# Kernel tuning notes

Hardware: AMD Instinct MI355X
Metric: run time of the kernel (lower is better)

The kernel has to match this reference:

```python
import jax, jax.numpy as jnp
import numpy as np
import math

B, L, H, E = 16, 1024, 8, 64   # L = nsensor = N (forced by einsum 'bhls,bhlg')
WIN = 1024                      # win_size, last dim of x
G = 64                          # n_group
D_SEL = 1                       # d_sel default


def setup_inputs() -> dict:
    key = jax.random.key(0)
    ks = jax.random.split(key, 7)
    return {
        "queries": jax.random.normal(ks[0], (B, L, H, E), dtype=jnp.float32),
        "keys": jax.random.normal(ks[1], (B, L, H, E), dtype=jnp.float32),
        "values": jax.random.normal(ks[2], (B, L, H, E), dtype=jnp.float32),
        "x": jax.random.normal(ks[3], (B, L, WIN), dtype=jnp.float32),
        "mlp_w": jax.random.normal(ks[4], (H * D_SEL, WIN), dtype=jnp.float32) * 0.02,
        "mlp_b": jax.random.normal(ks[5], (H * D_SEL,), dtype=jnp.float32) * 0.02,
        "sel_W": jax.random.normal(ks[6], (H, G, D_SEL), dtype=jnp.float32),
        "attn_mask": 0,
    }


def _select_attention(x, mlp_w, mlp_b, sel_W, n_heads, d_sel):
    b, n, lwin = x.shape
    xf = x.reshape(b * n, lwin)
    newx = jnp.tanh(xf @ mlp_w.T + mlp_b)                 # [(B*N), H*d_sel]
    # Faithful raw reshape (torch.reshape, no permute): mixes n and h axes.
    newx = newx.reshape(b, n_heads, n, d_sel)             # [B, H, N, d_sel]
    sel = jnp.einsum('bhnd,hgd->bhng', newx, sel_W)       # [B, H, N, G]
    return jax.nn.relu(sel)


def reference(queries, keys, values, x, mlp_w, mlp_b, sel_W, attn_mask):
    b, l, h, e = queries.shape
    scale = 1.0 / math.sqrt(e)
    scores = jnp.einsum('blhe,bshe->bhls', queries, keys)      # [B, H, L, S]
    sel = _select_attention(x, mlp_w, mlp_b, sel_W, h, D_SEL)  # [B, H, L, G]
    scores = jnp.einsum('bhls,bhlg->bhsg', scores, sel)        # [B, H, S, G]
    series = jax.nn.softmax(scale * scores, axis=-1)           # softmax over groups
    # values labeled 'blhs': l=S (value len), s=D (feature). Output V: [B, D, H, G]
    V = jnp.einsum('blhs,bhlg->bshg', values, series)
    return V
```

## Files before the change

kernel.cpp:

```cpp
#include <hip/hip_runtime.h>
#include <math.h>

#define NB 16
#define NL 1024
#define NH 8
#define NE 64
#define NWIN 1024
#define NG 64

#define SCH 128
#define SROW 136

typedef __attribute__((ext_vector_type(8))) short short8;
typedef __attribute__((ext_vector_type(4))) float floatx4;

__device__ __forceinline__ short f2bf(float x) {
    unsigned u = __float_as_uint(x);
    u += 0x7fffu + ((u >> 16) & 1u);
    return (short)(u >> 16);
}
__device__ __forceinline__ float dot4(float4 a, float4 b) {
    return fmaf(a.x, b.x, fmaf(a.y, b.y, fmaf(a.z, b.z, a.w * b.w)));
}

__global__ __launch_bounds__(256) void k_sel_q(
    const float* __restrict__ x, const float* __restrict__ mlp_w,
    const float* __restrict__ mlp_b, const float* __restrict__ q,
    float* __restrict__ qp, float* __restrict__ qn)
{
    __shared__ float4 w_lds[8][NWIN / 4];
    __shared__ float t_lds[256];
    __shared__ float redp[4][64], redn[4][64];

    int tid = threadIdx.x;
    int blk = blockIdx.x;
    int qq = blk & 3, bh = blk >> 2;
    int b = bh >> 3, h = bh & 7;
    int w = tid >> 6, lane = tid & 63;

    const float4* w4 = (const float4*)mlp_w;
    float4* wl = (float4*)w_lds;
    #pragma unroll
    for (int i = 0; i < 8; ++i)
        wl[tid + 256 * i] = w4[tid + 256 * i];
    __syncthreads();

    float4 keep03 = make_float4(0,0,0,0), keep47 = make_float4(0,0,0,0);
    int r0 = b * 1024 + h * 128 + qq * 32 + w * 8;
    for (int j = 0; j < 8; ++j) {
        const float4* xr = (const float4*)(x + (size_t)(r0 + j) * NWIN);
        float4 a03 = make_float4(0,0,0,0), a47 = make_float4(0,0,0,0);
        #pragma unroll
        for (int it = 0; it < 4; ++it) {
            float4 xv = xr[it * 64 + lane];
            a03.x += dot4(xv, w_lds[0][it * 64 + lane]);
            a03.y += dot4(xv, w_lds[1][it * 64 + lane]);
            a03.z += dot4(xv, w_lds[2][it * 64 + lane]);
            a03.w += dot4(xv, w_lds[3][it * 64 + lane]);
            a47.x += dot4(xv, w_lds[4][it * 64 + lane]);
            a47.y += dot4(xv, w_lds[5][it * 64 + lane]);
            a47.z += dot4(xv, w_lds[6][it * 64 + lane]);
            a47.w += dot4(xv, w_lds[7][it * 64 + lane]);
        }
        #pragma unroll
        for (int off = 1; off < 64; off <<= 1) {
            a03.x += __shfl_xor(a03.x, off, 64);
            a03.y += __shfl_xor(a03.y, off, 64);
            a03.z += __shfl_xor(a03.z, off, 64);
            a03.w += __shfl_xor(a03.w, off, 64);
            a47.x += __shfl_xor(a47.x, off, 64);
            a47.y += __shfl_xor(a47.y, off, 64);
            a47.z += __shfl_xor(a47.z, off, 64);
            a47.w += __shfl_xor(a47.w, off, 64);
        }
        if (lane == j) { keep03 = a03; keep47 = a47; }
    }
    if (lane < 8) {
        float4 b03 = *(const float4*)mlp_b;
        float4 b47 = *(const float4*)(mlp_b + 4);
        float4 t03, t47;
        t03.x = tanhf(keep03.x + b03.x); t03.y = tanhf(keep03.y + b03.y);
        t03.z = tanhf(keep03.z + b03.z); t03.w = tanhf(keep03.w + b03.w);
        t47.x = tanhf(keep47.x + b47.x); t47.y = tanhf(keep47.y + b47.y);
        t47.z = tanhf(keep47.z + b47.z); t47.w = tanhf(keep47.w + b47.w);
        *(float4*)&t_lds[w * 64 + lane * 8]     = t03;
        *(float4*)&t_lds[w * 64 + lane * 8 + 4] = t47;
    }
    __syncthreads();

    int lo = lane >> 4, e4 = lane & 15;
    float4 accp = make_float4(0,0,0,0), accn = make_float4(0,0,0,0);
    #pragma unroll 4
    for (int i = 0; i < 16; ++i) {
        int l_loc = w * 64 + i * 4 + lo;
        float tv = t_lds[l_loc];
        int l = qq * 256 + l_loc;
        float4 qv = *(const float4*)(q + (((size_t)(b * NL + l)) * NH + h) * NE + e4 * 4);
        float tp = fmaxf(tv, 0.f), tn = fminf(tv, 0.f);
        accp.x = fmaf(tp, qv.x, accp.x); accp.y = fmaf(tp, qv.y, accp.y);
        accp.z = fmaf(tp, qv.z, accp.z); accp.w = fmaf(tp, qv.w, accp.w);
        accn.x = fmaf(tn, qv.x, accn.x); accn.y = fmaf(tn, qv.y, accn.y);
        accn.z = fmaf(tn, qv.z, accn.z); accn.w = fmaf(tn, qv.w, accn.w);
    }
    #pragma unroll
    for (int off = 16; off <= 32; off <<= 1) {
        accp.x += __shfl_xor(accp.x, off, 64); accp.y += __shfl_xor(accp.y, off, 64);
        accp.z += __shfl_xor(accp.z, off, 64); accp.w += __shfl_xor(accp.w, off, 64);
        accn.x += __shfl_xor(accn.x, off, 64); accn.y += __shfl_xor(accn.y, off, 64);
        accn.z += __shfl_xor(accn.z, off, 64); accn.w += __shfl_xor(accn.w, off, 64);
    }
    if (lo == 0) {
        *(float4*)&redp[w][e4 * 4] = accp;
        *(float4*)&redn[w][e4 * 4] = accn;
    }
    __syncthreads();
    if (tid < 64) {
        atomicAdd(&qp[bh * NE + tid], redp[0][tid] + redp[1][tid] + redp[2][tid] + redp[3][tid]);
    } else if (tid < 128) {
        int e = tid - 64;
        atomicAdd(&qn[bh * NE + e], redn[0][e] + redn[1][e] + redn[2][e] + redn[3][e]);
    }
}

__global__ __launch_bounds__(256, 4) void k_attn_out(
    const float* __restrict__ keys, const float* __restrict__ values,
    const float* __restrict__ sel_W,
    const float* __restrict__ qp, const float* __restrict__ qn,
    float* __restrict__ out)
{
    __shared__ short sb[NG][SROW];
    __shared__ float ap_l[SCH], an_l[SCH];
    __shared__ float2 wpn[NG];
    __shared__ float mx2[2][SCH], dn2[2][SCH];

    int tid = threadIdx.x, blk = blockIdx.x;
    int chunk = blk & 7, bh = blk >> 3;
    int b = bh >> 3, h = bh & 7;
    int w = tid >> 6, lane = tid & 63;
    int c = lane & 15, sq = lane >> 4;
    const float scale = 0.125f;

    if (tid < NG) {
        float W = sel_W[h * NG + tid];
        wpn[tid] = make_float2(fmaxf(W, 0.f) * scale, fminf(W, 0.f) * scale);
    }

    const float4 qp4 = *(const float4*)(qp + bh * NE + c * 4);
    const float4 qn4 = *(const float4*)(qn + bh * NE + c * 4);
    int s0 = chunk * SCH;

    #pragma unroll
    for (int p = 0; p < 8; ++p) {
        int sl = w * 32 + p * 4 + sq;
        float4 kv = *(const float4*)(keys + (((size_t)(b * NL + s0 + sl)) * NH + h) * NE + c * 4);
        float pp = dot4(kv, qp4);
        float pn = dot4(kv, qn4);
        #pragma unroll
        for (int m_ = 1; m_ <= 8; m_ <<= 1) {
            pp += __shfl_xor(pp, m_, 64);
            pn += __shfl_xor(pn, m_, 64);
        }
        if (c == 0) { ap_l[sl] = pp; an_l[sl] = pn; }
    }
    __syncthreads();

    {
        int s_ = tid & 127, gh = tid >> 7, g0 = gh * 32;
        float ap = ap_l[s_], an = an_l[s_];
        float m = -1e30f;
        #pragma unroll 8
        for (int g = 0; g < 32; ++g) {
            float2 wv = wpn[g0 + g];
            m = fmaxf(m, fmaf(wv.x, ap, wv.y * an));
        }
        mx2[gh][s_] = m;
        __syncthreads();
        m = fmaxf(mx2[0][s_], mx2[1][s_]);
        float d = 0.f;
        #pragma unroll 8
        for (int g = 0; g < 32; ++g) {
            float2 wv = wpn[g0 + g];
            d += __expf(fmaf(wv.x, ap, wv.y * an) - m);
        }
        dn2[gh][s_] = d;
        __syncthreads();
        float inv = 1.0f / (dn2[0][s_] + dn2[1][s_]);
        #pragma unroll 8
        for (int g = 0; g < 32; ++g) {
            float2 wv = wpn[g0 + g];
            sb[g0 + g][s_] = f2bf(__expf(fmaf(wv.x, ap, wv.y * an) - m) * inv);
        }
    }
    __syncthreads();

    floatx4 acc[4] = {{0.f,0.f,0.f,0.f},{0.f,0.f,0.f,0.f},
                      {0.f,0.f,0.f,0.f},{0.f,0.f,0.f,0.f}};
    const float* vbase = values + (((size_t)(b * NL + s0)) * NH + h) * NE + 16 * w + c;
    #pragma unroll
    for (int ks = 0; ks < 4; ++ks) {
        float a[8];
        #pragma unroll
        for (int j = 0; j < 8; ++j)
            a[j] = vbase[(size_t)(ks * 32 + sq * 8 + j) * (NH * NE)];
        short8 av;
        #pragma unroll
        for (int j = 0; j < 8; ++j) av[j] = f2bf(a[j]);
        #pragma unroll
        for (int n = 0; n < 4; ++n) {
            short8 bv = *(const short8*)&sb[16 * n + c][ks * 32 + sq * 8];
            acc[n] = __builtin_amdgcn_mfma_f32_16x16x32_bf16(av, bv, acc[n], 0, 0, 0);
        }
    }

    #pragma unroll
    for (int n = 0; n < 4; ++n) {
        #pragma unroll
        for (int r = 0; r < 4; ++r) {
            int e = 16 * w + sq * 4 + r;
            int g = 16 * n + c;
            atomicAdd(&out[((size_t)(b * NE + e) * NH + h) * NG + g], acc[n][r]);
        }
    }
}

extern "C" void kernel_launch(void* const* d_in, const int* in_sizes, int n_in,
                              void* d_out, int out_size, void* d_ws, size_t ws_size,
                              hipStream_t stream) {
    (void)in_sizes; (void)n_in; (void)ws_size;
    const float* queries = (const float*)d_in[0];
    const float* keys    = (const float*)d_in[1];
    const float* values  = (const float*)d_in[2];
    const float* x       = (const float*)d_in[3];
    const float* mlp_w   = (const float*)d_in[4];
    const float* mlp_b   = (const float*)d_in[5];
    const float* sel_W   = (const float*)d_in[6];
    float* out = (float*)d_out;

    float* qp_ws = (float*)d_ws;
    float* qn_ws = qp_ws + NB * NH * NE;

    hipMemsetAsync(out, 0, (size_t)out_size * sizeof(float), stream);
    hipMemsetAsync(qp_ws, 0, (size_t)2 * NB * NH * NE * sizeof(float), stream);

    k_sel_q<<<dim3(NB * NH * 4), dim3(256), 0, stream>>>(x, mlp_w, mlp_b,
                                                          queries, qp_ws, qn_ws);
    k_attn_out<<<dim3(NB * NH * 8), dim3(256), 0, stream>>>(keys, values, sel_W,
                                                            qp_ws, qn_ws, out);
}
```

Before: 199.2 us.

## Double grid of selection kernel, prefetch values, replace output atomics with partial-sum reduction

The selection/MLP kernel now launches twice as many blocks, each covering half the rows. It double-buffers x row loads and uses a transpose-style butterfly reduction so each lane ends up with one output instead of reducing all eight. The attention kernel issues its value loads at kernel start to overlap them with the softmax work. It writes per-chunk partial outputs instead of atomically adding to the output, and a new reduce kernel sums the eight chunks. This removes the output memset and atomics but adds a workspace round trip, an extra launch and higher register pressure from 32 prefetched floats.

```diff
diff --git a/kernel.cpp b/kernel.cpp
--- a/kernel.cpp
+++ b/kernel.cpp
@@ -29,12 +29,12 @@
     float* __restrict__ qp, float* __restrict__ qn)
 {
     __shared__ float4 w_lds[8][NWIN / 4];
-    __shared__ float t_lds[256];
+    __shared__ float t_lds[128];
     __shared__ float redp[4][64], redn[4][64];
 
     int tid = threadIdx.x;
     int blk = blockIdx.x;
-    int qq = blk & 3, bh = blk >> 2;
+    int qq = blk & 7, bh = blk >> 3;
     int b = bh >> 3, h = bh & 7;
     int w = tid >> 6, lane = tid & 63;
 
@@ -45,56 +45,63 @@
         wl[tid + 256 * i] = w4[tid + 256 * i];
     __syncthreads();
 
-    float4 keep03 = make_float4(0,0,0,0), keep47 = make_float4(0,0,0,0);
-    int r0 = b * 1024 + h * 128 + qq * 32 + w * 8;
-    for (int j = 0; j < 8; ++j) {
-        const float4* xr = (const float4*)(x + (size_t)(r0 + j) * NWIN);
-        float4 a03 = make_float4(0,0,0,0), a47 = make_float4(0,0,0,0);
+    int r0 = b * 1024 + h * 128 + qq * 16 + w * 4;
+    float bc = mlp_b[lane & 7];
+    float4 xa[4], xb[4];
+    {
+        const float4* p0 = (const float4*)(x + (size_t)r0 * NWIN);
+        #pragma unroll
+        for (int it = 0; it < 4; ++it) xa[it] = p0[it * 64 + lane];
+    }
+    #pragma unroll
+    for (int j = 0; j < 4; ++j) {
+        if (j < 3) {
+            const float4* pn = (const float4*)(x + (size_t)(r0 + j + 1) * NWIN);
+            #pragma unroll
+            for (int it = 0; it < 4; ++it) xb[it] = pn[it * 64 + lane];
+        }
+        float o0=0,o1=0,o2=0,o3=0,o4=0,o5=0,o6=0,o7=0;
         #pragma unroll
         for (int it = 0; it < 4; ++it) {
-            float4 xv = xr[it * 64 + lane];
-            a03.x += dot4(xv, w_lds[0][it * 64 + lane]);
-            a03.y += dot4(xv, w_lds[1][it * 64 + lane]);
-            a03.z += dot4(xv, w_lds[2][it * 64 + lane]);
-            a03.w += dot4(xv, w_lds[3][it * 64 + lane]);
-            a47.x += dot4(xv, w_lds[4][it * 64 + lane]);
-            a47.y += dot4(xv, w_lds[5][it * 64 + lane]);
-            a47.z += dot4(xv, w_lds[6][it * 64 + lane]);
-            a47.w += dot4(xv, w_lds[7][it * 64 + lane]);
-        }
-        #pragma unroll
-        for (int off = 1; off < 64; off <<= 1) {
-            a03.x += __shfl_xor(a03.x, off, 64);
-            a03.y += __shfl_xor(a03.y, off, 64);
-            a03.z += __shfl_xor(a03.z, off, 64);
-            a03.w += __shfl_xor(a03.w, off, 64);
-            a47.x += __shfl_xor(a47.x, off, 64);
-            a47.y += __shfl_xor(a47.y, off, 64);
-            a47.z += __shfl_xor(a47.z, off, 64);
-            a47.w += __shfl_xor(a47.w, off, 64);
-        }
-        if (lane == j) { keep03 = a03; keep47 = a47; }
-    }
-    if (lane < 8) {
-        float4 b03 = *(const float4*)mlp_b;
-        float4 b47 = *(const float4*)(mlp_b + 4);
-        float4 t03, t47;
-        t03.x = tanhf(keep03.x + b03.x); t03.y = tanhf(keep03.y + b03.y);
-        t03.z = tanhf(keep03.z + b03.z); t03.w = tanhf(keep03.w + b03.w);
-        t47.x = tanhf(keep47.x + b47.x); t47.y = tanhf(keep47.y + b47.y);
-        t47.z = tanhf(keep47.z + b47.z); t47.w = tanhf(keep47.w + b47.w);
-        *(float4*)&t_lds[w * 64 + lane * 8]     = t03;
-        *(float4*)&t_lds[w * 64 + lane * 8 + 4] = t47;
-    }
-    __syncthreads();
+            float4 xv = xa[it];
+            o0 += dot4(xv, w_lds[0][it * 64 + lane]);
+            o1 += dot4(xv, w_lds[1][it * 64 + lane]);
+            o2 += dot4(xv, w_lds[2][it * 64 + lane]);
+            o3 += dot4(xv, w_lds[3][it * 64 + lane]);
+            o4 += dot4(xv, w_lds[4][it * 64 + lane]);
+            o5 += dot4(xv, w_lds[5][it * 64 + lane]);
+            o6 += dot4(xv, w_lds[6][it * 64 + lane]);
+            o7 += dot4(xv, w_lds[7][it * 64 + lane]);
+        }
+        o0 += __shfl_xor(o0, 1, 64); o1 += __shfl_xor(o1, 1, 64);
+        o2 += __shfl_xor(o2, 1, 64); o3 += __shfl_xor(o3, 1, 64);
+        o4 += __shfl_xor(o4, 1, 64); o5 += __shfl_xor(o5, 1, 64);
+        o6 += __shfl_xor(o6, 1, 64); o7 += __shfl_xor(o7, 1, 64);
+        bool b0 = lane & 1;
+        float m0 = b0 ? o1 : o0, m1 = b0 ? o3 : o2;
+        float m2 = b0 ? o5 : o4, m3 = b0 ? o7 : o6;
+        m0 += __shfl_xor(m0, 2, 64); m1 += __shfl_xor(m1, 2, 64);
+        m2 += __shfl_xor(m2, 2, 64); m3 += __shfl_xor(m3, 2, 64);
+        bool b1 = lane & 2;
+        float n0 = b1 ? m1 : m0, n1 = b1 ? m3 : m2;
+        n0 += __shfl_xor(n0, 4, 64); n1 += __shfl_xor(n1, 4, 64);
+        float q0 = (lane & 4) ? n1 : n0;
+        q0 += __shfl_xor(q0, 8, 64);
+        q0 += __shfl_xor(q0, 16, 64);
+        q0 += __shfl_xor(q0, 32, 64);
+        if (lane < 8)
+            t_lds[w * 32 + j * 8 + lane] = tanhf(q0 + bc);
+        #pragma unroll
+        for (int it = 0; it < 4; ++it) xa[it] = xb[it];
+    }
 
     int lo = lane >> 4, e4 = lane & 15;
     float4 accp = make_float4(0,0,0,0), accn = make_float4(0,0,0,0);
-    #pragma unroll 4
-    for (int i = 0; i < 16; ++i) {
-        int l_loc = w * 64 + i * 4 + lo;
+    #pragma unroll
+    for (int i = 0; i < 8; ++i) {
+        int l_loc = w * 32 + i * 4 + lo;
         float tv = t_lds[l_loc];
-        int l = qq * 256 + l_loc;
+        int l = qq * 128 + l_loc;
         float4 qv = *(const float4*)(q + (((size_t)(b * NL + l)) * NH + h) * NE + e4 * 4);
         float tp = fmaxf(tv, 0.f), tn = fminf(tv, 0.f);
         accp.x = fmaf(tp, qv.x, accp.x); accp.y = fmaf(tp, qv.y, accp.y);
@@ -126,7 +133,7 @@
     const float* __restrict__ keys, const float* __restrict__ values,
     const float* __restrict__ sel_W,
     const float* __restrict__ qp, const float* __restrict__ qn,
-    float* __restrict__ out)
+    float* __restrict__ partial)
 {
     __shared__ short sb[NG][SROW];
     __shared__ float ap_l[SCH], an_l[SCH];
@@ -139,15 +146,22 @@
     int w = tid >> 6, lane = tid & 63;
     int c = lane & 15, sq = lane >> 4;
     const float scale = 0.125f;
+    int s0 = chunk * SCH;
+
+    float vreg[32];
+    const float* vbase = values + (((size_t)(b * NL + s0)) * NH + h) * NE + 16 * w + c;
+    #pragma unroll
+    for (int ks = 0; ks < 4; ++ks)
+        #pragma unroll
+        for (int j = 0; j < 8; ++j)
+            vreg[ks * 8 + j] = vbase[(size_t)(ks * 32 + sq * 8 + j) * (NH * NE)];
 
     if (tid < NG) {
         float W = sel_W[h * NG + tid];
         wpn[tid] = make_float2(fmaxf(W, 0.f) * scale, fminf(W, 0.f) * scale);
     }
-
     const float4 qp4 = *(const float4*)(qp + bh * NE + c * 4);
     const float4 qn4 = *(const float4*)(qn + bh * NE + c * 4);
-    int s0 = chunk * SCH;
 
     #pragma unroll
     for (int p = 0; p < 8; ++p) {
@@ -195,16 +209,11 @@
 
     floatx4 acc[4] = {{0.f,0.f,0.f,0.f},{0.f,0.f,0.f,0.f},
                       {0.f,0.f,0.f,0.f},{0.f,0.f,0.f,0.f}};
-    const float* vbase = values + (((size_t)(b * NL + s0)) * NH + h) * NE + 16 * w + c;
     #pragma unroll
     for (int ks = 0; ks < 4; ++ks) {
-        float a[8];
-        #pragma unroll
-        for (int j = 0; j < 8; ++j)
-            a[j] = vbase[(size_t)(ks * 32 + sq * 8 + j) * (NH * NE)];
         short8 av;
         #pragma unroll
-        for (int j = 0; j < 8; ++j) av[j] = f2bf(a[j]);
+        for (int j = 0; j < 8; ++j) av[j] = f2bf(vreg[ks * 8 + j]);
         #pragma unroll
         for (int n = 0; n < 4; ++n) {
             short8 bv = *(const short8*)&sb[16 * n + c][ks * 32 + sq * 8];
@@ -212,21 +221,36 @@
         }
     }
 
+    float* pch = partial + (size_t)chunk * (NB * NE * NH * NG);
     #pragma unroll
     for (int n = 0; n < 4; ++n) {
         #pragma unroll
         for (int r = 0; r < 4; ++r) {
             int e = 16 * w + sq * 4 + r;
             int g = 16 * n + c;
-            atomicAdd(&out[((size_t)(b * NE + e) * NH + h) * NG + g], acc[n][r]);
-        }
-    }
+            pch[((size_t)(b * NE + e) * NH + h) * NG + g] = acc[n][r];
+        }
+    }
+}
+
+__global__ __launch_bounds__(256) void k_reduce(
+    const float* __restrict__ partial, float* __restrict__ out)
+{
+    int i = blockIdx.x * 256 + threadIdx.x;
+    const float4* p = (const float4*)partial;
+    float4 s = p[i];
+    #pragma unroll
+    for (int ch = 1; ch < 8; ++ch) {
+        float4 t = p[(size_t)ch * 131072 + i];
+        s.x += t.x; s.y += t.y; s.z += t.z; s.w += t.w;
+    }
+    ((float4*)out)[i] = s;
 }
 
 extern "C" void kernel_launch(void* const* d_in, const int* in_sizes, int n_in,
                               void* d_out, int out_size, void* d_ws, size_t ws_size,
                               hipStream_t stream) {
-    (void)in_sizes; (void)n_in; (void)ws_size;
+    (void)in_sizes; (void)n_in; (void)ws_size; (void)out_size;
     const float* queries = (const float*)d_in[0];
     const float* keys    = (const float*)d_in[1];
     const float* values  = (const float*)d_in[2];
@@ -236,14 +260,15 @@
     const float* sel_W   = (const float*)d_in[6];
     float* out = (float*)d_out;
 
-    float* qp_ws = (float*)d_ws;
+    float* partial = (float*)d_ws;
+    float* qp_ws = partial + 8 * (NB * NE * NH * NG);
     float* qn_ws = qp_ws + NB * NH * NE;
 
-    hipMemsetAsync(out, 0, (size_t)out_size * sizeof(float), stream);
     hipMemsetAsync(qp_ws, 0, (size_t)2 * NB * NH * NE * sizeof(float), stream);
 
-    k_sel_q<<<dim3(NB * NH * 4), dim3(256), 0, stream>>>(x, mlp_w, mlp_b,
+    k_sel_q<<<dim3(NB * NH * 8), dim3(256), 0, stream>>>(x, mlp_w, mlp_b,
                                                           queries, qp_ws, qn_ws);
     k_attn_out<<<dim3(NB * NH * 8), dim3(256), 0, stream>>>(keys, values, sel_W,
-                                                            qp_ws, qn_ws, out);
-}
+                                                            qp_ws, qn_ws, partial);
+    k_reduce<<<dim3(512), dim3(256), 0, stream>>>(partial, out);
+}
```

Result: no change. 202.7 us (+1.8%).
